# Kernel tuning notes

Hardware: AMD Instinct MI355X
Metric: run time of the kernel (lower is better)

Reference implementation:

```python
import jax, jax.numpy as jnp
import numpy as np

B, IMG, D, HEADS, L, PC, PF, OUT = 8, 128, 128, 4, 2, 8, 4, 32
HC = IMG // PC; NC = HC * HC          # 16x16 -> 256 coarse tokens
HF = IMG // PF; NF = HF * HF          # 32x32 -> 1024 fine tokens


def _ln(x, g, b):
    m = x.mean(-1, keepdims=True)
    v = x.var(-1, keepdims=True)
    return (x - m) * jax.lax.rsqrt(v + 1e-5) * g + b


def _conv(x, w, b, pad):
    y = jax.lax.conv_general_dilated(x, w, (1, 1), ((pad, pad), (pad, pad)),
                                     dimension_numbers=('NCHW', 'OIHW', 'NCHW'))
    return y + b[None, :, None, None]


def _bilinear_ac(x, oh, ow):  # F.interpolate(mode='bilinear', align_corners=True)
    _, _, H, W = x.shape
    ys = jnp.linspace(0.0, H - 1.0, oh)
    xs = jnp.linspace(0.0, W - 1.0, ow)
    y0 = jnp.floor(ys).astype(jnp.int32); y1 = jnp.minimum(y0 + 1, H - 1); wy = (ys - y0)[:, None]
    x0 = jnp.floor(xs).astype(jnp.int32); x1 = jnp.minimum(x0 + 1, W - 1); wx = (xs - x0)[None, :]
    g = lambda yi, xi: x[:, :, yi][:, :, :, xi]
    return (g(y0, x0) * (1 - wy) * (1 - wx) + g(y0, x1) * (1 - wy) * wx
            + g(y1, x0) * wy * (1 - wx) + g(y1, x1) * wy * wx)


def _patchify(x, p):  # F.unfold with kernel=stride=p, in_chans=1
    b, _, h, w = x.shape
    return x.reshape(b, h // p, p, w // p, p).transpose(0, 1, 3, 2, 4).reshape(b, (h // p) * (w // p), p * p)


def _forward(x, Wpc, bpc, Wpf, bpf, type_embed, ln1_g, ln1_b, Wqkv, Wo, bo,
             ln2_g, ln2_b, W1, b1, W2, b2, dWc, dbc, dWf, dbf, fW1, fb1, fW2, fb2):
    Bx = x.shape[0]
    # ---- multi-scale patch embed ----
    coarse = _patchify(x, PC) @ Wpc + bpc + type_embed[0]   # [B,NC,D]
    fine = _patchify(x, PF) @ Wpf + bpf                     # [B,NF,D]
    # ---- edge map: sobel -> avgpool(4) -> threshold at per-image mean ----
    gray = x.mean(1, keepdims=True)
    kx = jnp.array([[[[-1, 0, 1], [-2, 0, 2], [-1, 0, 1]]]], x.dtype)
    ky = jnp.array([[[[-1, -2, -1], [0, 0, 0], [1, 2, 1]]]], x.dtype)
    sx = _conv(gray, kx, jnp.zeros((1,), x.dtype), 1)
    sy = _conv(gray, ky, jnp.zeros((1,), x.dtype), 1)
    e = jnp.sqrt(sx ** 2 + sy ** 2)
    e = e.reshape(Bx, 1, IMG // 4, 4, IMG // 4, 4).mean((3, 5))  # [B,1,32,32] == fine grid
    mask_flat = (e > e.mean((2, 3), keepdims=True)).reshape(Bx, NF)
    # ---- static-shape analogue of per-sample masked gather + pad_sequence:
    # stable sort puts edge tokens first (original pixel order preserved), pads are zeros
    order = jnp.argsort(jnp.logical_not(mask_flat), axis=1, stable=True)   # [B,NF]
    mask_sorted = jnp.take_along_axis(mask_flat, order, 1)
    fine_sorted = jnp.take_along_axis(fine, order[..., None], 1) * mask_sorted[..., None]
    fine_sorted = fine_sorted + type_embed[1]   # type embed added to pads too (as in torch)
    tokens = jnp.concatenate([coarse, fine_sorted], axis=1)   # [B,N,D]
    N = NC + NF
    hd = D // HEADS
    scale = hd ** -0.5
    # ---- encoder blocks (pre-LN attn + MLP, irregular-token path) ----
    for l in range(L):
        y = _ln(tokens, ln1_g[l], ln1_b[l])
        qkv = (y @ Wqkv[l]).reshape(Bx, N, 3, HEADS, hd).transpose(2, 0, 3, 1, 4)
        q, k, v = qkv[0], qkv[1], qkv[2]
        attn = jax.nn.softmax(jnp.einsum('bhqd,bhkd->bhqk', q, k) * scale, axis=-1)
        o = jnp.einsum('bhqk,bhkd->bhqd', attn, v).transpose(0, 2, 1, 3).reshape(Bx, N, D)
        tokens = tokens + o @ Wo[l] + bo[l]
        y = _ln(tokens, ln2_g[l], ln2_b[l])
        tokens = tokens + jax.nn.gelu(y @ W1[l] + b1[l], approximate=False) @ W2[l] + b2[l]
    # ---- multi-scale decoder ----
    c = (tokens[:, :NC] @ dWc + dbc).reshape(Bx, HC, HC, 1).transpose(0, 3, 1, 2)
    c_up = _bilinear_ac(c, OUT, OUT)
    feats = (tokens[:, NC:] @ dWf + dbf) * mask_sorted[..., None]   # pads stay zero
    inv = jnp.argsort(order, axis=1)                                # scatter back to pixel order
    f_flat = jnp.take_along_axis(feats, inv[..., None], 1)          # [B,NF,1]
    f_map = f_flat.reshape(Bx, HF, HF, 1).transpose(0, 3, 1, 2)
    f_up = _bilinear_ac(f_map, OUT, OUT)
    fused = jnp.concatenate([c_up, f_up], axis=1)
    h = jax.nn.relu(_conv(fused, fW1, fb1, 1))
    return _conv(h, fW2, fb2, 1)   # [B,1,32,32]


def setup_inputs() -> dict:
    key = jax.random.key(0)
    ks = jax.random.split(key, 16)
    n = lambda k, shape: jax.random.normal(k, shape, jnp.float32) * 0.02
    z = lambda *shape: jnp.zeros(shape, jnp.float32)
    return {
        'x': jax.random.normal(ks[0], (B, 1, IMG, IMG), jnp.float32),
        'Wpc': n(ks[1], (PC * PC, D)), 'bpc': z(D),
        'Wpf': n(ks[2], (PF * PF, D)), 'bpf': z(D),
        'type_embed': n(ks[3], (2, D)),
        'ln1_g': jnp.ones((L, D), jnp.float32), 'ln1_b': z(L, D),
        'Wqkv': n(ks[4], (L, D, 3 * D)),
        'Wo': n(ks[5], (L, D, D)), 'bo': z(L, D),
        'ln2_g': jnp.ones((L, D), jnp.float32), 'ln2_b': z(L, D),
        'W1': n(ks[6], (L, D, 2 * D)), 'b1': z(L, 2 * D),
        'W2': n(ks[7], (L, 2 * D, D)), 'b2': z(L, D),
        'dWc': n(ks[8], (D, 1)), 'dbc': z(1),
        'dWf': n(ks[9], (D, 1)), 'dbf': z(1),
        'fW1': n(ks[10], (2, 2, 3, 3)) * 10.0, 'fb1': z(2),
        'fW2': n(ks[11], (1, 2, 3, 3)) * 10.0, 'fb2': z(1),
    }


def reference(x, Wpc, bpc, Wpf, bpf, type_embed, ln1_g, ln1_b, Wqkv, Wo, bo,
              ln2_g, ln2_b, W1, b1, W2, b2, dWc, dbc, dWf, dbf, fW1, fb1, fW2, fb2):
    return _forward(x, Wpc, bpc, Wpf, bpf, type_embed, ln1_g, ln1_b, Wqkv, Wo, bo,
                    ln2_g, ln2_b, W1, b1, W2, b2, dWc, dbc, dWf, dbf, fW1, fb1, fW2, fb2)
```

## Files before the change

### kernel.cpp

```cpp
#include <hip/hip_runtime.h>
#include <math.h>

#define Bx 8
#define IMG 128
#define DD 128
#define HEADS 4
#define LL 2
#define PCc 8
#define PFf 4
#define HCc 16
#define NCc 256
#define HFf 32
#define NFf 1024
#define NTOK 1280
#define HD 32
#define SPLIT 2
#define NSTG 10
#define NQT 20

typedef __attribute__((ext_vector_type(8))) short short8;
typedef __attribute__((ext_vector_type(4))) float f32x4;

__device__ __forceinline__ short f2bf(float f) {
  unsigned u = __builtin_bit_cast(unsigned, f);
  u += 0x7FFF + ((u >> 16) & 1);
  return (short)(u >> 16);
}
__device__ __forceinline__ float bf2f(short s) {
  unsigned u = ((unsigned)(unsigned short)s) << 16;
  return __builtin_bit_cast(float, u);
}

__global__ __launch_bounds__(256) void k_prologue(const float* __restrict__ x,
    const float* __restrict__ Wpc, const float* __restrict__ bpc,
    const float* __restrict__ Wpf, const float* __restrict__ bpf,
    const float* __restrict__ te,
    const float* __restrict__ Wqkv, const float* __restrict__ Wo,
    const float* __restrict__ W1, const float* __restrict__ W2,
    short* __restrict__ WtQKV, short* __restrict__ WtO,
    short* __restrict__ Wt1, short* __restrict__ Wt2,
    float* __restrict__ e, float* __restrict__ tokens,
    float* __restrict__ fineb) {
  int blk = blockIdx.x;
  int t = threadIdx.x;
  if (blk < 1024) {
    int idx = blk * 256 + t;
    int l = idx / 131072, r = idx % 131072;
    const float* src; short* dst; int N, off;
    if (r < 49152)      { src = Wqkv + l * 49152; dst = WtQKV + l * 49152; N = 384; off = r; }
    else if (r < 65536) { src = Wo + l * 16384;  dst = WtO + l * 16384;  N = 128; off = r - 49152; }
    else if (r < 98304) { src = W1 + l * 32768;  dst = Wt1 + l * 32768;  N = 256; off = r - 65536; }
    else                { src = W2 + l * 32768;  dst = Wt2 + l * 32768;  N = 128; off = r - 98304; }
    int k = off / N, n = off % N;
    int K = (r >= 98304) ? 256 : 128;
    dst[(size_t)n * K + k] = f2bf(src[off]);
  } else if (blk < 1536) {
    int bt = blk - 1024;
    int b = bt >> 6, tile = bt & 63;
    int ty = tile >> 3, tx = tile & 7;
    int ly = t >> 4, lx = t & 15;
    int py = ty * 16 + ly, px = tx * 16 + lx;
    const float* img = x + (size_t)b * IMG * IMG;
    float v[3][3];
    #pragma unroll
    for (int ky = 0; ky < 3; ++ky)
      #pragma unroll
      for (int kx = 0; kx < 3; ++kx) {
        int yy = py + ky - 1, xx = px + kx - 1;
        v[ky][kx] = (yy >= 0 && yy < IMG && xx >= 0 && xx < IMG)
                        ? img[yy * IMG + xx] : 0.f;
      }
    float gx = -v[0][0] + v[0][2] - 2.f * v[1][0] + 2.f * v[1][2] - v[2][0] + v[2][2];
    float gy = -v[0][0] - 2.f * v[0][1] - v[0][2] + v[2][0] + 2.f * v[2][1] + v[2][2];
    __shared__ float sm[256];
    sm[t] = sqrtf(gx * gx + gy * gy);
    __syncthreads();
    if (t < 16) {
      int cy = t >> 2, cx = t & 3;
      float s = 0.f;
      #pragma unroll
      for (int dy = 0; dy < 4; ++dy)
        #pragma unroll
        for (int dx = 0; dx < 4; ++dx) s += sm[(cy * 4 + dy) * 16 + cx * 4 + dx];
      e[b * NFf + (ty * 4 + cy) * 32 + tx * 4 + cx] = s * (1.f / 16.f);
    }
  } else if (blk < 2560) {
    int bt = (blk - 1536) * 2 + (t >> 7);
    int b = bt / NCc, tok = bt % NCc;
    int hc = tok / HCc, wc = tok % HCc;
    int half = t >> 7, d = t & 127;
    __shared__ float patch[2][PCc * PCc];
    if (d < PCc * PCc) {
      int pi = d / PCc, pj = d % PCc;
      patch[half][d] = x[(b * IMG + hc * PCc + pi) * IMG + wc * PCc + pj];
    }
    __syncthreads();
    float acc = bpc[d] + te[d];
    #pragma unroll 8
    for (int i = 0; i < PCc * PCc; ++i) acc += patch[half][i] * Wpc[i * DD + d];
    tokens[(size_t)(b * NTOK + tok) * DD + d] = acc;
  } else {
    int ft = (blk - 2560) * 2 + (t >> 7);
    int b = ft >> 10, tloc = ft & 1023;
    int hf = tloc >> 5, wf = tloc & 31;
    int half = t >> 7, d = t & 127;
    __shared__ float patch[2][PFf * PFf];
    if (d < PFf * PFf) {
      int pi = d / PFf, pj = d % PFf;
      patch[half][d] = x[(b * IMG + hf * PFf + pi) * IMG + wf * PFf + pj];
    }
    __syncthreads();
    float acc = bpf[d];
    #pragma unroll
    for (int i = 0; i < PFf * PFf; ++i) acc += patch[half][i] * Wpf[i * DD + d];
    fineb[(size_t)(b * NFf + tloc) * DD + d] = acc;
  }
}

__global__ __launch_bounds__(1024) void k_edge_sort(const float* __restrict__ e,
    int* __restrict__ order, float* __restrict__ msort) {
  int b = blockIdx.x;
  int t = threadIdx.x;
  int lane = t & 63, wave = t >> 6;
  float ev = e[b * NFf + t];
  __shared__ float wsum[16];
  __shared__ int wcnt[16];
  float r = ev;
  #pragma unroll
  for (int o = 32; o > 0; o >>= 1) r += __shfl_xor(r, o, 64);
  if (lane == 0) wsum[wave] = r;
  __syncthreads();
  float tot = 0.f;
  #pragma unroll
  for (int i = 0; i < 16; ++i) tot += wsum[i];
  float mean = tot * (1.f / 1024.f);
  int m = (ev > mean) ? 1 : 0;
  unsigned long long bal = __ballot(m);
  if (lane == 0) wcnt[wave] = __popcll(bal);
  __syncthreads();
  int wbase = 0, total = 0;
  #pragma unroll
  for (int i = 0; i < 16; ++i) {
    int c = wcnt[i];
    if (i < wave) wbase += c;
    total += c;
  }
  unsigned long long below = (lane == 63) ? ~0ULL : ((1ULL << (lane + 1)) - 1);
  int incl = __popcll(bal & below);
  int eb = wbase + incl - m;
  int pos = m ? eb : (total + t - eb);
  order[b * NFf + pos] = t;
  msort[b * NFf + pos] = (float)m;
}

__global__ __launch_bounds__(256) void k_gather_qkv(float* __restrict__ tokens,
    const float* __restrict__ fineb, const int* __restrict__ order,
    const float* __restrict__ msort, const float* __restrict__ te,
    const float* __restrict__ g, const float* __restrict__ bb,
    const short* __restrict__ WtQ, short* __restrict__ qkvb) {
  __shared__ short Blds[128 * 128];
  __shared__ short Ylds[32 * 136];
  int row0 = blockIdx.x * 32;
  int t = threadIdx.x;
  int lane = t & 63, w = t >> 6;
  int m = lane & 15, quad = lane >> 4;
  int rt = w >> 1, ch = w & 1;
  int lrow = lane >> 4, jphys = lane & 15;
  f32x4 zero = {0.f, 0.f, 0.f, 0.f};

  #pragma unroll
  for (int j = 0; j < 8; ++j) {
    int c = j * 4 + w;
    int r = c * 4 + lrow;
    int jlog = jphys ^ (r & 15);
    __builtin_amdgcn_global_load_lds(
        (const unsigned*)&WtQ[(size_t)r * 128 + jlog * 8],
        (unsigned*)&Blds[c * 512], 16, 0, 0);
  }
  float2 gg = ((const float2*)g)[lane];
  float2 bv = ((const float2*)bb)[lane];
  #pragma unroll
  for (int rr = 0; rr < 8; ++rr) {
    int lr = w * 8 + rr;
    int row = row0 + lr;
    int b = row / NTOK, rl = row % NTOK;
    float2 v;
    if (rl < NCc) {
      v = ((const float2*)(tokens + (size_t)row * DD))[lane];
    } else {
      int pos = rl - NCc;
      int src = order[b * NFf + pos];
      float mk = msort[b * NFf + pos];
      float2 u = ((const float2*)(fineb + (size_t)(b * NFf + src) * DD))[lane];
      float2 tv = ((const float2*)(te + DD))[lane];
      v.x = u.x * mk + tv.x;
      v.y = u.y * mk + tv.y;
      ((float2*)(tokens + (size_t)row * DD))[lane] = v;
    }
    float s = v.x + v.y;
    #pragma unroll
    for (int o = 32; o > 0; o >>= 1) s += __shfl_xor(s, o, 64);
    float mean = s * (1.f / 128.f);
    float cx = v.x - mean, cy = v.y - mean;
    float q = cx * cx + cy * cy;
    #pragma unroll
    for (int o = 32; o > 0; o >>= 1) q += __shfl_xor(q, o, 64);
    float rstd = rsqrtf(q * (1.f / 128.f) + 1e-5f);
    int p = (int)(unsigned short)f2bf(cx * rstd * gg.x + bv.x)
          | ((int)(unsigned short)f2bf(cy * rstd * gg.y + bv.y) << 16);
    ((int*)Ylds)[lr * 68 + lane] = p;
  }
  for (int c3 = 0; c3 < 3; ++c3) {
    if (c3) {
      __syncthreads();
      #pragma unroll
      for (int j = 0; j < 8; ++j) {
        int c = j * 4 + w;
        int r = c * 4 + lrow;
        int jlog = jphys ^ (r & 15);
        __builtin_amdgcn_global_load_lds(
            (const unsigned*)&WtQ[(size_t)(c3 * 128 + r) * 128 + jlog * 8],
            (unsigned*)&Blds[c * 512], 16, 0, 0);
      }
    }
    __syncthreads();
    f32x4 qa[4] = {zero, zero, zero, zero};
    #pragma unroll
    for (int ks = 0; ks < 4; ++ks) {
      short8 af = *(const short8*)&Ylds[(rt * 16 + m) * 136 + quad * 8 + ks * 32];
      int pc = ((quad + ks * 4) ^ m) * 8;
      #pragma unroll
      for (int nt = 0; nt < 4; ++nt) {
        short8 bf = *(const short8*)&Blds[(ch * 64 + nt * 16 + m) * 128 + pc];
        qa[nt] = __builtin_amdgcn_mfma_f32_16x16x32_bf16(af, bf, qa[nt], 0, 0, 0);
      }
    }
    #pragma unroll
    for (int nt = 0; nt < 4; ++nt) {
      int col = c3 * 128 + ch * 64 + nt * 16 + m;
      #pragma unroll
      for (int r = 0; r < 4; ++r) {
        int row = row0 + rt * 16 + quad * 4 + r;
        qkvb[(size_t)row * 384 + col] = f2bf(qa[nt][r]);
      }
    }
  }
}

__global__ __launch_bounds__(256) void k_fused(const short* __restrict__ Opart,
    const float* __restrict__ Lpart, const short* __restrict__ WtO,
    const float* __restrict__ bo_, const float* __restrict__ ln2g_,
    const float* __restrict__ ln2b_, const short* __restrict__ Wt1,
    const float* __restrict__ b1_, const short* __restrict__ Wt2,
    const float* __restrict__ b2_, float* __restrict__ tokens,
    const float* __restrict__ ln1g_, const float* __restrict__ ln1b_,
    const short* __restrict__ WtQ, short* __restrict__ qkvb,
    const float* __restrict__ dWc_, const float* __restrict__ dbc_,
    const float* __restrict__ dWf_, const float* __restrict__ dbf_,
    float* __restrict__ hrow) {
  __shared__ short Blds[128 * 128];
  __shared__ short AH[32 * 268];
  __shared__ short Ylds[32 * 136];
  __shared__ float pls[2][32], plq[2][32];
  int row0 = blockIdx.x * 32;
  int b = row0 / NTOK;
  int rloc = row0 % NTOK;
  int qt = rloc >> 6, qoff = rloc & 63;
  int t = threadIdx.x;
  int lane = t & 63, w = t >> 6;
  int m = lane & 15, quad = lane >> 4;
  int rt = w >> 1, ch = w & 1;
  int lrow = lane >> 4, jphys = lane & 15;
  f32x4 zero = {0.f, 0.f, 0.f, 0.f};

  #pragma unroll
  for (int j = 0; j < 8; ++j) {
    int c = j * 4 + w;
    int r = c * 4 + lrow;
    int jlog = jphys ^ (r & 15);
    __builtin_amdgcn_global_load_lds(
        (const unsigned*)&WtO[(size_t)r * 128 + jlog * 8],
        (unsigned*)&Blds[c * 512], 16, 0, 0);
  }
  #pragma unroll
  for (int it = 0; it < 2; ++it) {
    int idx = t + it * 256;
    int q = idx >> 4, j = idx & 15;
    int dh = j >> 2, dd = (j & 3) * 8;
    int qg = qoff + q;
    size_t pb = ((size_t)(b * HEADS + dh) * NQT + qt) * SPLIT;
    float L = 0.f;
    #pragma unroll
    for (int sk = 0; sk < SPLIT; ++sk) L += Lpart[(pb + sk) * 64 + qg];
    float o[8] = {0, 0, 0, 0, 0, 0, 0, 0};
    #pragma unroll
    for (int sk = 0; sk < SPLIT; ++sk) {
      short8 po = *(const short8*)&Opart[(pb + sk) * 2048 + qg * 32 + dd];
      #pragma unroll
      for (int i = 0; i < 8; ++i) o[i] += bf2f(po[i]);
    }
    float rs = 1.f / L;
    short8 ov;
    #pragma unroll
    for (int i = 0; i < 8; ++i) ov[i] = f2bf(o[i] * rs);
    *(short8*)&AH[q * 136 + j * 8] = ov;
  }
  __syncthreads();
  f32x4 acc[4] = {zero, zero, zero, zero};
  #pragma unroll
  for (int ks = 0; ks < 4; ++ks) {
    short8 af = *(const short8*)&AH[(rt * 16 + m) * 136 + quad * 8 + ks * 32];
    int pc = ((quad + ks * 4) ^ m) * 8;
    #pragma unroll
    for (int nt = 0; nt < 4; ++nt) {
      short8 bf = *(const short8*)&Blds[(ch * 64 + nt * 16 + m) * 128 + pc];
      acc[nt] = __builtin_amdgcn_mfma_f32_16x16x32_bf16(af, bf, acc[nt], 0, 0, 0);
    }
  }
  float v[4][4];
  #pragma unroll
  for (int nt = 0; nt < 4; ++nt) {
    int col = ch * 64 + nt * 16 + m;
    float bv = bo_[col];
    #pragma unroll
    for (int r = 0; r < 4; ++r) {
      int row = row0 + rt * 16 + quad * 4 + r;
      v[nt][r] = acc[nt][r] + bv + tokens[(size_t)row * DD + col];
    }
  }
  #pragma unroll
  for (int r = 0; r < 4; ++r) {
    float s = v[0][r] + v[1][r] + v[2][r] + v[3][r];
    float q = v[0][r] * v[0][r] + v[1][r] * v[1][r]
            + v[2][r] * v[2][r] + v[3][r] * v[3][r];
    #pragma unroll
    for (int o = 1; o < 16; o <<= 1) { s += __shfl_xor(s, o); q += __shfl_xor(q, o); }
    if (m == 0) {
      int lr = rt * 16 + quad * 4 + r;
      pls[ch][lr] = s;
      plq[ch][lr] = q;
    }
  }
  __syncthreads();
  #pragma unroll
  for (int j = 0; j < 8; ++j) {
    int c = j * 4 + w;
    int r = c * 4 + lrow;
    int jlog = jphys ^ (r & 15);
    __builtin_amdgcn_global_load_lds(
        (const unsigned*)&Wt1[(size_t)r * 128 + jlog * 8],
        (unsigned*)&Blds[c * 512], 16, 0, 0);
  }
  #pragma unroll
  for (int r = 0; r < 4; ++r) {
    int lr = rt * 16 + quad * 4 + r;
    float S = pls[0][lr] + pls[1][lr];
    float Q = plq[0][lr] + plq[1][lr];
    float mean = S * (1.f / 128.f);
    float var = Q * (1.f / 128.f) - mean * mean;
    float rstd = rsqrtf(var + 1e-5f);
    #pragma unroll
    for (int nt = 0; nt < 4; ++nt) {
      int col = ch * 64 + nt * 16 + m;
      Ylds[lr * 136 + col] = f2bf((v[nt][r] - mean) * rstd * ln2g_[col] + ln2b_[col]);
    }
  }
  for (int hh = 0; hh < 2; ++hh) {
    if (hh) {
      __syncthreads();
      #pragma unroll
      for (int j = 0; j < 8; ++j) {
        int c = j * 4 + w;
        int r = c * 4 + lrow;
        int jlog = jphys ^ (r & 15);
        __builtin_amdgcn_global_load_lds(
            (const unsigned*)&Wt1[(size_t)(128 + r) * 128 + jlog * 8],
            (unsigned*)&Blds[c * 512], 16, 0, 0);
      }
    }
    __syncthreads();
    f32x4 ha[4] = {zero, zero, zero, zero};
    #pragma unroll
    for (int ks = 0; ks < 4; ++ks) {
      short8 af = *(const short8*)&Ylds[(rt * 16 + m) * 136 + quad * 8 + ks * 32];
      int pc = ((quad + ks * 4) ^ m) * 8;
      #pragma unroll
      for (int nt = 0; nt < 4; ++nt) {
        short8 bf = *(const short8*)&Blds[(ch * 64 + nt * 16 + m) * 128 + pc];
        ha[nt] = __builtin_amdgcn_mfma_f32_16x16x32_bf16(af, bf, ha[nt], 0, 0, 0);
      }
    }
    #pragma unroll
    for (int nt = 0; nt < 4; ++nt) {
      int n = hh * 128 + ch * 64 + nt * 16 + m;
      float bv = b1_[n];
      #pragma unroll
      for (int r = 0; r < 4; ++r) {
        float vv = ha[nt][r] + bv;
        vv = 0.5f * vv * (1.f + erff(vv * 0.70710678118654752f));
        AH[(rt * 16 + quad * 4 + r) * 268 + n] = f2bf(vv);
      }
    }
  }
  f32x4 a2[4] = {zero, zero, zero, zero};
  for (int kb = 0; kb < 2; ++kb) {
    __syncthreads();
    #pragma unroll
    for (int j = 0; j < 8; ++j) {
      int c = j * 4 + w;
      int r = c * 4 + lrow;
      int jlog = jphys ^ (r & 15);
      __builtin_amdgcn_global_load_lds(
          (const unsigned*)&Wt2[(size_t)r * 256 + kb * 128 + jlog * 8],
          (unsigned*)&Blds[c * 512], 16, 0, 0);
    }
    __syncthreads();
    #pragma unroll
    for (int ks = 0; ks < 4; ++ks) {
      int pc = ((quad + ks * 4) ^ m) * 8;
      short8 af = *(const short8*)&AH[(rt * 16 + m) * 268 + kb * 128
                                      + quad * 8 + ks * 32];
      #pragma unroll
      for (int nt = 0; nt < 4; ++nt) {
        short8 bf = *(const short8*)&Blds[(ch * 64 + nt * 16 + m) * 128 + pc];
        a2[nt] = __builtin_amdgcn_mfma_f32_16x16x32_bf16(af, bf, a2[nt], 0, 0, 0);
      }
    }
  }
  #pragma unroll
  for (int nt = 0; nt < 4; ++nt) {
    int col = ch * 64 + nt * 16 + m;
    float bv = b2_[col];
    #pragma unroll
    for (int r = 0; r < 4; ++r) {
      int row = row0 + rt * 16 + quad * 4 + r;
      float val = a2[nt][r] + bv + v[nt][r];
      tokens[(size_t)row * DD + col] = val;
      v[nt][r] = val;
    }
  }
  if (ln1g_ == nullptr) {
    bool coarse = (rloc < NCc);
    const float* dw = coarse ? dWc_ : dWf_;
    float dwv[4];
    #pragma unroll
    for (int nt = 0; nt < 4; ++nt) dwv[nt] = dw[ch * 64 + nt * 16 + m];
    #pragma unroll
    for (int r = 0; r < 4; ++r) {
      float s = v[0][r] * dwv[0] + v[1][r] * dwv[1]
              + v[2][r] * dwv[2] + v[3][r] * dwv[3];
      #pragma unroll
      for (int o = 1; o < 16; o <<= 1) s += __shfl_xor(s, o);
      if (m == 0) pls[ch][rt * 16 + quad * 4 + r] = s;
    }
    __syncthreads();
    if (m == 0 && ch == 0) {
      float dbv = coarse ? dbc_[0] : dbf_[0];
      #pragma unroll
      for (int r = 0; r < 4; ++r) {
        int lr = rt * 16 + quad * 4 + r;
        hrow[row0 + lr] = pls[0][lr] + pls[1][lr] + dbv;
      }
    }
    return;
  }
  #pragma unroll
  for (int r = 0; r < 4; ++r) {
    float s = v[0][r] + v[1][r] + v[2][r] + v[3][r];
    float q = v[0][r] * v[0][r] + v[1][r] * v[1][r]
            + v[2][r] * v[2][r] + v[3][r] * v[3][r];
    #pragma unroll
    for (int o = 1; o < 16; o <<= 1) { s += __shfl_xor(s, o); q += __shfl_xor(q, o); }
    if (m == 0) {
      int lr = rt * 16 + quad * 4 + r;
      pls[ch][lr] = s;
      plq[ch][lr] = q;
    }
  }
  __syncthreads();
  #pragma unroll
  for (int j = 0; j < 8; ++j) {
    int c = j * 4 + w;
    int r = c * 4 + lrow;
    int jlog = jphys ^ (r & 15);
    __builtin_amdgcn_global_load_lds(
        (const unsigned*)&WtQ[(size_t)r * 128 + jlog * 8],
        (unsigned*)&Blds[c * 512], 16, 0, 0);
  }
  #pragma unroll
  for (int r = 0; r < 4; ++r) {
    int lr = rt * 16 + quad * 4 + r;
    float S = pls[0][lr] + pls[1][lr];
    float Q = plq[0][lr] + plq[1][lr];
    float mean = S * (1.f / 128.f);
    float var = Q * (1.f / 128.f) - mean * mean;
    float rstd = rsqrtf(var + 1e-5f);
    #pragma unroll
    for (int nt = 0; nt < 4; ++nt) {
      int col = ch * 64 + nt * 16 + m;
      Ylds[lr * 136 + col] = f2bf((v[nt][r] - mean) * rstd * ln1g_[col] + ln1b_[col]);
    }
  }
  for (int c3 = 0; c3 < 3; ++c3) {
    if (c3) {
      __syncthreads();
      #pragma unroll
      for (int j = 0; j < 8; ++j) {
        int c = j * 4 + w;
        int r = c * 4 + lrow;
        int jlog = jphys ^ (r & 15);
        __builtin_amdgcn_global_load_lds(
            (const unsigned*)&WtQ[(size_t)(c3 * 128 + r) * 128 + jlog * 8],
            (unsigned*)&Blds[c * 512], 16, 0, 0);
      }
    }
    __syncthreads();
    f32x4 qa[4] = {zero, zero, zero, zero};
    #pragma unroll
    for (int ks = 0; ks < 4; ++ks) {
      short8 af = *(const short8*)&Ylds[(rt * 16 + m) * 136 + quad * 8 + ks * 32];
      int pc = ((quad + ks * 4) ^ m) * 8;
      #pragma unroll
      for (int nt = 0; nt < 4; ++nt) {
        short8 bf = *(const short8*)&Blds[(ch * 64 + nt * 16 + m) * 128 + pc];
        qa[nt] = __builtin_amdgcn_mfma_f32_16x16x32_bf16(af, bf, qa[nt], 0, 0, 0);
      }
    }
    #pragma unroll
    for (int nt = 0; nt < 4; ++nt) {
      int col = c3 * 128 + ch * 64 + nt * 16 + m;
      #pragma unroll
      for (int r = 0; r < 4; ++r) {
        int row = row0 + rt * 16 + quad * 4 + r;
        qkvb[(size_t)row * 384 + col] = f2bf(qa[nt][r]);
      }
    }
  }
}

__global__ __launch_bounds__(256) void k_attn4(const short* __restrict__ qkv,
    short* __restrict__ Opart, float* __restrict__ Lpart) {
  __shared__ short Ks[64 * 32];
  __shared__ short Vt[32 * 74];
  __shared__ short Pl[4][16 * 74];

  int sk = blockIdx.x % SPLIT;
  int qt = (blockIdx.x / SPLIT) % NQT;
  int h  = (blockIdx.x / (SPLIT * NQT)) % HEADS;
  int b  = blockIdx.x / (SPLIT * NQT * HEADS);
  int t = threadIdx.x;
  int lane = t & 63, w = t >> 6;
  int m = lane & 15, quad = lane >> 4;
  int q0 = qt * 64 + w * 16;

  const float scale = 0.17677669529663687f;
  short8 qraw = *(const short8*)(qkv + ((size_t)(b * NTOK) + q0 + m) * 384 + h * HD + quad * 8);
  short8 qf;
  #pragma unroll
  for (int j = 0; j < 8; ++j) qf[j] = f2bf(bf2f(qraw[j]) * scale);

  f32x4 zero = {0.f, 0.f, 0.f, 0.f};
  f32x4 Oacc[2] = {zero, zero};
  float psum[4] = {0.f, 0.f, 0.f, 0.f};

  int skey = t >> 2, sdseg = t & 3;
  int jlogK = sdseg ^ ((skey >> 1) & 3);
  const short* kstage = qkv + ((size_t)(b * NTOK) + skey) * 384 + 128 + h * HD + jlogK * 8;
  const short* vstage = qkv + ((size_t)(b * NTOK) + skey) * 384 + 256 + h * HD + sdseg * 8;
  int kswz = (quad ^ ((m >> 1) & 3)) * 8;

  for (int s = sk * NSTG; s < sk * NSTG + NSTG; ++s) {
    __syncthreads();
    __builtin_amdgcn_global_load_lds((const unsigned*)(kstage + (size_t)s * 64 * 384),
                                     (unsigned*)&Ks[w * 512], 16, 0, 0);
    short8 vf = *(const short8*)(vstage + (size_t)s * 64 * 384);
    #pragma unroll
    for (int j = 0; j < 8; ++j) Vt[(sdseg * 8 + j) * 74 + skey] = vf[j];
    __syncthreads();

    f32x4 sc[4];
    #pragma unroll
    for (int ct = 0; ct < 4; ++ct) {
      short8 kfrag = *(const short8*)&Ks[(ct * 16 + m) * 32 + kswz];
      sc[ct] = __builtin_amdgcn_mfma_f32_16x16x32_bf16(qf, kfrag, zero, 0, 0, 0);
    }
    #pragma unroll
    for (int ct = 0; ct < 4; ++ct)
      #pragma unroll
      for (int r = 0; r < 4; ++r) {
        float p = __expf(sc[ct][r]);
        unsigned u = __builtin_bit_cast(unsigned, p);
        psum[r] += __builtin_bit_cast(float, u & 0xffff0000u);
        Pl[w][(quad * 4 + r) * 74 + ct * 16 + m] = (short)(u >> 16);
      }
    #pragma unroll
    for (int ks = 0; ks < 2; ++ks) {
      short8 pfrag = *(const short8*)&Pl[w][m * 74 + ks * 32 + quad * 8];
      #pragma unroll
      for (int nt = 0; nt < 2; ++nt) {
        short8 vfrag = *(const short8*)&Vt[(nt * 16 + m) * 74 + ks * 32 + quad * 8];
        Oacc[nt] = __builtin_amdgcn_mfma_f32_16x16x32_bf16(pfrag, vfrag, Oacc[nt], 0, 0, 0);
      }
    }
  }
  #pragma unroll
  for (int r = 0; r < 4; ++r) {
    float ssum = psum[r];
    #pragma unroll
    for (int o = 1; o < 16; o <<= 1) ssum += __shfl_xor(ssum, o);
    int qloc = w * 16 + quad * 4 + r;
    #pragma unroll
    for (int nt = 0; nt < 2; ++nt)
      Opart[(size_t)blockIdx.x * 2048 + qloc * 32 + nt * 16 + m] = f2bf(Oacc[nt][r]);
    if (m == 0) Lpart[(size_t)blockIdx.x * 64 + qloc] = ssum;
  }
}

__global__ __launch_bounds__(1024) void k_decoder(const float* __restrict__ hrow,
    const float* __restrict__ msort, const int* __restrict__ order,
    const float* __restrict__ fW1, const float* __restrict__ fb1,
    const float* __restrict__ fW2, const float* __restrict__ fb2,
    float* __restrict__ outp) {
  int b = blockIdx.x;
  int t = threadIdx.x;
  __shared__ float cmap[NCc];
  __shared__ float fmap[1024];
  __shared__ float cup[1024];
  __shared__ float hb[2][1024];
  fmap[order[b * NFf + t]] = hrow[b * NTOK + NCc + t] * msort[b * NFf + t];
  if (t < NCc) cmap[t] = hrow[b * NTOK + t];
  __syncthreads();
  int y = t >> 5, x = t & 31;
  {
    float ys = y * (15.f / 31.f);
    float xs = x * (15.f / 31.f);
    int y0 = (int)floorf(ys); int y1 = min(y0 + 1, 15); float wy = ys - (float)y0;
    int x0 = (int)floorf(xs); int x1 = min(x0 + 1, 15); float wx = xs - (float)x0;
    cup[t] = cmap[y0 * 16 + x0] * (1.f - wy) * (1.f - wx)
           + cmap[y0 * 16 + x1] * (1.f - wy) * wx
           + cmap[y1 * 16 + x0] * wy * (1.f - wx)
           + cmap[y1 * 16 + x1] * wy * wx;
  }
  __syncthreads();
  for (int oc = 0; oc < 2; ++oc) {
    float a = fb1[oc];
    #pragma unroll
    for (int ic = 0; ic < 2; ++ic)
      #pragma unroll
      for (int ky = 0; ky < 3; ++ky)
        #pragma unroll
        for (int kx = 0; kx < 3; ++kx) {
          int yy = y + ky - 1, xx = x + kx - 1;
          float v = 0.f;
          if (yy >= 0 && yy < 32 && xx >= 0 && xx < 32)
            v = ic == 0 ? cup[yy * 32 + xx] : fmap[yy * 32 + xx];
          a += v * fW1[((oc * 2 + ic) * 3 + ky) * 3 + kx];
        }
    hb[oc][t] = fmaxf(a, 0.f);
  }
  __syncthreads();
  float a = fb2[0];
  #pragma unroll
  for (int ic = 0; ic < 2; ++ic)
    #pragma unroll
    for (int ky = 0; ky < 3; ++ky)
      #pragma unroll
      for (int kx = 0; kx < 3; ++kx) {
        int yy = y + ky - 1, xx = x + kx - 1;
        float v = (yy >= 0 && yy < 32 && xx >= 0 && xx < 32)
                      ? hb[ic][yy * 32 + xx] : 0.f;
        a += v * fW2[(ic * 3 + ky) * 3 + kx];
      }
  outp[b * 1024 + t] = a;
}

extern "C" void kernel_launch(void* const* d_in, const int* in_sizes, int n_in,
                              void* d_out, int out_size, void* d_ws, size_t ws_size,
                              hipStream_t stream) {
  const float* x    = (const float*)d_in[0];
  const float* Wpc  = (const float*)d_in[1];
  const float* bpc  = (const float*)d_in[2];
  const float* Wpf  = (const float*)d_in[3];
  const float* bpf  = (const float*)d_in[4];
  const float* te   = (const float*)d_in[5];
  const float* ln1g = (const float*)d_in[6];
  const float* ln1b = (const float*)d_in[7];
  const float* Wqkv = (const float*)d_in[8];
  const float* Wo   = (const float*)d_in[9];
  const float* bo   = (const float*)d_in[10];
  const float* ln2g = (const float*)d_in[11];
  const float* ln2b = (const float*)d_in[12];
  const float* W1   = (const float*)d_in[13];
  const float* b1   = (const float*)d_in[14];
  const float* W2   = (const float*)d_in[15];
  const float* b2   = (const float*)d_in[16];
  const float* dWc  = (const float*)d_in[17];
  const float* dbc  = (const float*)d_in[18];
  const float* dWf  = (const float*)d_in[19];
  const float* dbf  = (const float*)d_in[20];
  const float* fW1  = (const float*)d_in[21];
  const float* fb1  = (const float*)d_in[22];
  const float* fW2  = (const float*)d_in[23];
  const float* fb2  = (const float*)d_in[24];

  char* ws = (char*)d_ws;
  float* tokens = (float*)ws;                 ws += 1310720 * 4;
  float* fineb  = (float*)ws;                 ws += 1048576 * 4;
  short* qkvb   = (short*)ws;                 ws += 3932160 * 2;
  short* Opart  = (short*)ws;                 ws += (size_t)(Bx * HEADS * NQT * SPLIT) * 2048 * 2;
  float* Lpart  = (float*)ws;                 ws += (size_t)(Bx * HEADS * NQT * SPLIT) * 64 * 4;
  short* WtQKV  = (short*)ws;                 ws += 98304 * 2;
  short* WtO    = (short*)ws;                 ws += 32768 * 2;
  short* Wt1    = (short*)ws;                 ws += 65536 * 2;
  short* Wt2    = (short*)ws;                 ws += 65536 * 2;
  float* ebuf   = (float*)ws;                 ws += 8192 * 4;
  float* msort  = (float*)ws;                 ws += 8192 * 4;
  int*   order  = (int*)ws;                   ws += 8192 * 4;
  float* hrow   = (float*)ws;                 ws += 10240 * 4;

  const int M = Bx * NTOK;

  k_prologue<<<6656, 256, 0, stream>>>(x, Wpc, bpc, Wpf, bpf, te, Wqkv, Wo, W1, W2,
                                       WtQKV, WtO, Wt1, Wt2, ebuf, tokens, fineb);
  k_edge_sort<<<Bx, 1024, 0, stream>>>(ebuf, order, msort);
  k_gather_qkv<<<M / 32, 256, 0, stream>>>(tokens, fineb, order, msort, te,
                                           ln1g, ln1b, WtQKV, qkvb);

  k_attn4<<<Bx * HEADS * NQT * SPLIT, 256, 0, stream>>>(qkvb, Opart, Lpart);
  k_fused<<<M / 32, 256, 0, stream>>>(
      Opart, Lpart, WtO, bo, ln2g, ln2b,
      Wt1, b1, Wt2, b2, tokens,
      ln1g + DD, ln1b + DD, WtQKV + 49152, qkvb,
      nullptr, nullptr, nullptr, nullptr, nullptr);

  k_attn4<<<Bx * HEADS * NQT * SPLIT, 256, 0, stream>>>(qkvb, Opart, Lpart);
  k_fused<<<M / 32, 256, 0, stream>>>(
      Opart, Lpart, WtO + 16384, bo + DD, ln2g + DD, ln2b + DD,
      Wt1 + 32768, b1 + 256, Wt2 + 32768, b2 + DD, tokens,
      nullptr, nullptr, nullptr, nullptr,
      dWc, dbc, dWf, dbf, hrow);

  k_decoder<<<Bx, 1024, 0, stream>>>(hrow, msort, order,
                                     fW1, fb1, fW2, fb2, (float*)d_out);
}
```

Baseline: 221.2 us.

## Double-buffer K/V staging in attention and remap block order by batch-head

The attention kernel now keeps two LDS buffers for K and V. While the current tile is being computed, it prefetches the next tile's K (async global-to-LDS) and V (into registers, then transposed into LDS), so there is one barrier per stage instead of two. The block index is also remapped so consecutive blocks handle different batch-head groups, with a logical id kept so output locations stay unchanged. This aims to hide global load latency and spread memory traffic, at the cost of more LDS and register pressure.

```diff
diff --git a/kernel.cpp b/kernel.cpp
--- a/kernel.cpp
+++ b/kernel.cpp
@@ -540,14 +540,16 @@
 
 __global__ __launch_bounds__(256) void k_attn4(const short* __restrict__ qkv,
     short* __restrict__ Opart, float* __restrict__ Lpart) {
-  __shared__ short Ks[64 * 32];
-  __shared__ short Vt[32 * 74];
+  __shared__ short Ks[2][64 * 32];
+  __shared__ short Vt[2][32 * 74];
   __shared__ short Pl[4][16 * 74];
 
-  int sk = blockIdx.x % SPLIT;
-  int qt = (blockIdx.x / SPLIT) % NQT;
-  int h  = (blockIdx.x / (SPLIT * NQT)) % HEADS;
-  int b  = blockIdx.x / (SPLIT * NQT * HEADS);
+  int hid = blockIdx.x;
+  int g = hid & 31;
+  int k = hid >> 5;
+  int b = g >> 2, h = g & 3;
+  int qt = k / SPLIT, sk = k % SPLIT;
+  size_t lid = ((size_t)g * NQT + qt) * SPLIT + sk;
   int t = threadIdx.x;
   int lane = t & 63, w = t >> 6;
   int m = lane & 15, quad = lane >> 4;
@@ -569,19 +571,30 @@
   const short* vstage = qkv + ((size_t)(b * NTOK) + skey) * 384 + 256 + h * HD + sdseg * 8;
   int kswz = (quad ^ ((m >> 1) & 3)) * 8;
 
-  for (int s = sk * NSTG; s < sk * NSTG + NSTG; ++s) {
-    __syncthreads();
-    __builtin_amdgcn_global_load_lds((const unsigned*)(kstage + (size_t)s * 64 * 384),
-                                     (unsigned*)&Ks[w * 512], 16, 0, 0);
-    short8 vf = *(const short8*)(vstage + (size_t)s * 64 * 384);
-    #pragma unroll
-    for (int j = 0; j < 8; ++j) Vt[(sdseg * 8 + j) * 74 + skey] = vf[j];
-    __syncthreads();
+  int s0 = sk * NSTG;
+  __builtin_amdgcn_global_load_lds((const unsigned*)(kstage + (size_t)s0 * 64 * 384),
+                                   (unsigned*)&Ks[0][w * 512], 16, 0, 0);
+  {
+    short8 vf = *(const short8*)(vstage + (size_t)s0 * 64 * 384);
+    #pragma unroll
+    for (int j = 0; j < 8; ++j) Vt[0][(sdseg * 8 + j) * 74 + skey] = vf[j];
+  }
+  __syncthreads();
+
+  for (int i = 0; i < NSTG; ++i) {
+    int cur = i & 1;
+    short8 vf;
+    if (i + 1 < NSTG) {
+      __builtin_amdgcn_global_load_lds(
+          (const unsigned*)(kstage + (size_t)(s0 + i + 1) * 64 * 384),
+          (unsigned*)&Ks[cur ^ 1][w * 512], 16, 0, 0);
+      vf = *(const short8*)(vstage + (size_t)(s0 + i + 1) * 64 * 384);
+    }
 
     f32x4 sc[4];
     #pragma unroll
     for (int ct = 0; ct < 4; ++ct) {
-      short8 kfrag = *(const short8*)&Ks[(ct * 16 + m) * 32 + kswz];
+      short8 kfrag = *(const short8*)&Ks[cur][(ct * 16 + m) * 32 + kswz];
       sc[ct] = __builtin_amdgcn_mfma_f32_16x16x32_bf16(qf, kfrag, zero, 0, 0, 0);
     }
     #pragma unroll
@@ -598,10 +611,15 @@
       short8 pfrag = *(const short8*)&Pl[w][m * 74 + ks * 32 + quad * 8];
       #pragma unroll
       for (int nt = 0; nt < 2; ++nt) {
-        short8 vfrag = *(const short8*)&Vt[(nt * 16 + m) * 74 + ks * 32 + quad * 8];
+        short8 vfrag = *(const short8*)&Vt[cur][(nt * 16 + m) * 74 + ks * 32 + quad * 8];
         Oacc[nt] = __builtin_amdgcn_mfma_f32_16x16x32_bf16(pfrag, vfrag, Oacc[nt], 0, 0, 0);
       }
     }
+    if (i + 1 < NSTG) {
+      #pragma unroll
+      for (int j = 0; j < 8; ++j) Vt[cur ^ 1][(sdseg * 8 + j) * 74 + skey] = vf[j];
+    }
+    __syncthreads();
   }
   #pragma unroll
   for (int r = 0; r < 4; ++r) {
@@ -611,8 +629,8 @@
     int qloc = w * 16 + quad * 4 + r;
     #pragma unroll
     for (int nt = 0; nt < 2; ++nt)
-      Opart[(size_t)blockIdx.x * 2048 + qloc * 32 + nt * 16 + m] = f2bf(Oacc[nt][r]);
-    if (m == 0) Lpart[(size_t)blockIdx.x * 64 + qloc] = ssum;
+      Opart[lid * 2048 + qloc * 32 + nt * 16 + m] = f2bf(Oacc[nt][r]);
+    if (m == 0) Lpart[lid * 64 + qloc] = ssum;
   }
 }
 
```

After: 218.4 us. No clear change (-1.2%).
